# Kernel tuning notes

Hardware: AMD Instinct MI355X
Metric: run time of the kernel (lower is better)

Reference implementation:

```python
import jax, jax.numpy as jnp
import numpy as np

I, L, T, S = 128, 8, 128, 128   # input neurons, topo batches, neurons per batch, fan-in span
BIG = 1e9
EPS = 1e-5


def setup_inputs() -> dict:
    key = jax.random.key(0)
    ks = jax.random.split(key, 7)
    x = jax.random.normal(ks[0], (I,), jnp.float32)
    # per-neuron weights|bias, scaled down for numerical stability of softmax/gelu chain
    W = jax.random.normal(ks[1], (L, T, S + 1), jnp.float32) * 0.05
    mask = (jax.random.uniform(ks[2], (L, T, S)) > 0.5).astype(jnp.float32)  # DAG connectivity
    attn_t = jax.random.normal(ks[3], (L, 3, S, S + 1), jnp.float32) * 0.05      # topo q/k/v (weight|bias)
    attn_n = jax.random.normal(ks[4], (L, T, 3, S, S + 1), jnp.float32) * 0.05   # per-neuron q/k/v
    # additive attention mask: attend only over a neuron's actual inputs
    attn_mask_n = BIG * (1.0 - mask[:, :, :, None] * mask[:, :, None, :])        # (L,T,S,S)
    norm_params = jnp.stack([jnp.ones((L, S)), jnp.zeros((L, S))], 1) \
        + 0.1 * jax.random.normal(ks[5], (L, 2, S), jnp.float32)                 # gamma, beta
    ada = jnp.ones((L, T, 2), jnp.float32) \
        + 0.1 * jax.random.normal(ks[6], (L, T, 2), jnp.float32)                 # gain, amplification
    span_ids = jnp.arange(L * S, dtype=jnp.int32).reshape(L, S)    # gather indices per topo batch
    tb_ids = I + jnp.arange(L * T, dtype=jnp.int32).reshape(L, T)  # scatter indices per topo batch
    return dict(x=x, W=W, mask=mask, attn_t=attn_t, attn_n=attn_n,
                attn_mask_n=attn_mask_n, norm_params=norm_params, ada=ada,
                span_ids=span_ids, tb_ids=tb_ids)


def _attention(qkv, vals, amask):
    # qkv: (3, S, S+1) stacked query/key/value (weight|bias); vals: (S,)
    wq, bq = qkv[0, :, :-1], qkv[0, :, -1]
    wk, bk = qkv[1, :, :-1], qkv[1, :, -1]
    wv, bv = qkv[2, :, :-1], qkv[2, :, -1]
    q = wq @ vals + bq
    k = wk @ vals + bk
    v = wv @ vals + bv
    scores = jnp.outer(q, k) * jax.lax.rsqrt(jnp.float32(vals.shape[0])) - amask
    return jax.nn.softmax(scores) @ v + vals  # residual connection


def _forward(x, W, mask, attn_t, attn_n, attn_mask_n, norm_params, ada, span_ids, tb_ids):
    values = jnp.zeros((I + L * T,), x.dtype).at[jnp.arange(I)].set(x)
    for b in range(L):  # fixed, small topological batch order
        vals = values[span_ids[b]]                                  # gather fan-in span (S,)
        mu = jnp.mean(vals)
        var = jnp.var(vals)
        vals = (vals - mu) * jax.lax.rsqrt(var + EPS)               # topo norm (standardize)
        vals = vals * norm_params[b, 0] + norm_params[b, 1]
        vals = _attention(attn_t[b], vals, 0.0)                     # topo-level self-attention
        # neuron-level self-attention, vmapped over the batch's T neurons -> (T, S)
        vals_n = jax.vmap(_attention, in_axes=(0, None, 0))(attn_n[b], vals, attn_mask_n[b])
        w, bias = W[b, :, :-1], W[b, :, -1]
        aff = jnp.einsum('ts,ts->t', w * mask[b], vals_n) + bias    # masked affine per neuron
        if b == L - 1:
            out = aff                                               # output neurons: identity transform
        else:
            out = jax.nn.gelu(aff * ada[b, :, 0]) * ada[b, :, 1]    # adaptive activation a*sigma(b*x)
        values = values.at[tb_ids[b]].set(out)
    return values[tb_ids[L - 1]]


def reference(x, W, mask, attn_t, attn_n, attn_mask_n, norm_params, ada, span_ids, tb_ids):
    return _forward(x, W, mask, attn_t, attn_n, attn_mask_n, norm_params, ada, span_ids, tb_ids)
```

## Files before the change

### kernel.cpp

```cpp
#include <hip/hip_runtime.h>
#include <math.h>

#define L_DIM 8
#define T_DIM 128
#define S_DIM 128
#define SP1   129
#define NSTRIDE 132
#define BIGF  1000000000.0f
#define EPSF  1e-5f
#define NTHREADS 1024
#define NWAVES 16

template<int CTRL>
__device__ __forceinline__ float dpp_add_part(float x) {
    int r = __builtin_amdgcn_update_dpp(0, __float_as_int(x), CTRL, 0xF, 0xF, false);
    return __int_as_float(r);
}
__device__ __forceinline__ float dpp16Sum15(float x) {
    x += dpp_add_part<0x111>(x);
    x += dpp_add_part<0x112>(x);
    x += dpp_add_part<0x114>(x);
    x += dpp_add_part<0x118>(x);
    return x;
}
__device__ __forceinline__ float dppSum63(float x) {
    x += dpp_add_part<0x111>(x);
    x += dpp_add_part<0x112>(x);
    x += dpp_add_part<0x114>(x);
    x += dpp_add_part<0x118>(x);
    x += dpp_add_part<0x142>(x);
    x += dpp_add_part<0x143>(x);
    return x;
}
__device__ __forceinline__ float lane63(float x) {
    return __int_as_float(__builtin_amdgcn_readlane(__float_as_int(x), 63));
}

__device__ __forceinline__ void wg_bar() {
    asm volatile("s_waitcnt lgkmcnt(0)" ::: "memory");
    __builtin_amdgcn_s_barrier();
    asm volatile("" ::: "memory");
}

__device__ __forceinline__ void gld_lds4(const float* g, float* l) {
    __builtin_amdgcn_global_load_lds(
        (const __attribute__((address_space(1))) void*)g,
        (__attribute__((address_space(3))) void*)l,
        4, 0, 0);
}

__device__ __forceinline__ void mv_glb4(const float* __restrict__ mat,
                                        const float in[8], int li, int rb,
                                        float* __restrict__ dst) {
#pragma unroll
    for (int p = 0; p < 4; ++p) {
        int r = rb + 4 * p;
        const float* row = mat + (size_t)r * SP1;
        float acc = 0.0f;
#pragma unroll
        for (int e = 0; e < 8; ++e) acc = fmaf(row[li * 8 + e], in[e], acc);
        acc = dpp16Sum15(acc);
        if (li == 15) dst[r] = acc + row[128];
    }
}

__device__ __forceinline__ void mv_stage2(const float* __restrict__ mat,
                                          const float* __restrict__ biasArr,
                                          const float in[8], int li, int r_base,
                                          float* __restrict__ dst) {
#pragma unroll
    for (int p = 0; p < 2; ++p) {
        int r = r_base + p * 4;
        const float* row = mat + r * NSTRIDE;
        float acc = 0.0f;
#pragma unroll
        for (int e = 0; e < 8; ++e) acc = fmaf(row[li * 8 + e], in[e], acc);
        acc = dpp16Sum15(acc);
        if (li == 15) dst[r] = acc + biasArr[r];
    }
}

__device__ __forceinline__ void mv_regs(const float wv[2][8], const float wb[2],
                                        const float in[8], int li, int r_base,
                                        float* __restrict__ dst) {
#pragma unroll
    for (int p = 0; p < 2; ++p) {
        float acc = 0.0f;
#pragma unroll
        for (int e = 0; e < 8; ++e) acc = fmaf(wv[p][e], in[e], acc);
        acc = dpp16Sum15(acc);
        if (li == 15) dst[r_base + p * 4] = acc + wb[p];
    }
}

__device__ __forceinline__ void attn_sm_t(int li, int r_base,
                                          const float* __restrict__ lds_q,
                                          const float* __restrict__ lds_k,
                                          const float* __restrict__ lds_v,
                                          const float* __restrict__ resid,
                                          float* __restrict__ lds_out)
{
    const float scale = 0.08838834764831845f;
    float kx[8], vx[8];
#pragma unroll
    for (int e = 0; e < 8; ++e) { kx[e] = lds_k[li * 8 + e]; vx[e] = lds_v[li * 8 + e]; }
#pragma unroll
    for (int p = 0; p < 2; ++p) {
        int r = r_base + p * 4;
        float qs = lds_q[r] * scale;
        float den = 0.0f, num = 0.0f;
#pragma unroll
        for (int e = 0; e < 8; ++e) {
            float ee = __expf(qs * kx[e]);
            den += ee;
            num = fmaf(ee, vx[e], num);
        }
        den = dpp16Sum15(den);
        num = dpp16Sum15(num);
        if (li == 15) lds_out[r] = num / den + resid[r];
    }
}

__global__ __launch_bounds__(NTHREADS)
void net_kernel(const float* __restrict__ x,
                const float* __restrict__ W,
                const float* __restrict__ maskp,
                const float* __restrict__ attn_t,
                const float* __restrict__ attn_n,
                const float* __restrict__ norm_params,
                const float* __restrict__ ada,
                float* __restrict__ out,
                unsigned long long* __restrict__ mbox)
{
    const int t    = blockIdx.x;
    const int tid  = threadIdx.x;
    const int lane = tid & 63;
    const int wid  = tid >> 6;
    const int li   = lane & 15;
    const int g    = lane >> 4;
    const int r0   = wid * 8 + g;
    const int r1   = r0 + 4;

    __shared__ float lds_nq[S_DIM * NSTRIDE];
    __shared__ float lds_nk[S_DIM * NSTRIDE];
    __shared__ float lds_nqb[S_DIM], lds_nkb[S_DIM];
    __shared__ float lds_vals[S_DIM];
    __shared__ float lds_q[S_DIM], lds_k[S_DIM], lds_v[S_DIM];
    __shared__ float lds_tv[S_DIM];
    __shared__ float lds_aff[NWAVES];

    float nv[2][8];
    float nvb0, nvb1;

    {
        const float* srcn = attn_n + (size_t)t * 3 * S_DIM * SP1;
        if (wid >= 8) {
            if (wid == 8)  gld_lds4(srcn + (size_t)lane * SP1 + 128, lds_nqb);
            if (wid == 9)  gld_lds4(srcn + (size_t)(64 + lane) * SP1 + 128, lds_nqb + 64);
            if (wid == 10) gld_lds4(srcn + (size_t)(S_DIM + lane) * SP1 + 128, lds_nkb);
            if (wid == 11) gld_lds4(srcn + (size_t)(S_DIM + 64 + lane) * SP1 + 128, lds_nkb + 64);
            const float* kb_ = srcn + S_DIM * SP1;
#pragma unroll
            for (int k2 = 0; k2 < 16; ++k2) {
                int r = (wid - 8) + 8 * k2;
                gld_lds4(srcn + (size_t)r * SP1 + lane,      lds_nq + r * NSTRIDE);
                gld_lds4(srcn + (size_t)r * SP1 + 64 + lane, lds_nq + r * NSTRIDE + 64);
                gld_lds4(kb_  + (size_t)r * SP1 + lane,      lds_nk + r * NSTRIDE);
                gld_lds4(kb_  + (size_t)r * SP1 + 64 + lane, lds_nk + r * NSTRIDE + 64);
            }
        }
        const float* vb_ = srcn + 2 * S_DIM * SP1;
#pragma unroll
        for (int e = 0; e < 8; ++e) {
            nv[0][e] = vb_[(size_t)r0 * SP1 + li * 8 + e];
            nv[1][e] = vb_[(size_t)r1 * SP1 + li * 8 + e];
        }
        nvb0 = vb_[(size_t)r0 * SP1 + 128];
        nvb1 = vb_[(size_t)r1 * SP1 + 128];
    }

    for (int b = 0; b < L_DIM; ++b) {
        if (wid == 0) {
            float np00 = norm_params[(b * 2 + 0) * S_DIM + lane];
            float np10 = norm_params[(b * 2 + 0) * S_DIM + lane + 64];
            float np01 = norm_params[(b * 2 + 1) * S_DIM + lane];
            float np11 = norm_params[(b * 2 + 1) * S_DIM + lane + 64];
            float v0, v1;
            if (b == 0) {
                v0 = x[lane]; v1 = x[lane + 64];
            } else {
                float a00 = ada[((b - 1) * T_DIM + lane) * 2 + 0];
                float a01 = ada[((b - 1) * T_DIM + lane) * 2 + 1];
                float a10 = ada[((b - 1) * T_DIM + lane + 64) * 2 + 0];
                float a11 = ada[((b - 1) * T_DIM + lane + 64) * 2 + 1];
                const unsigned long long* mb_ = mbox + (size_t)(b - 1) * T_DIM;
                unsigned long long u0, u1;
                do {
                    u0 = __hip_atomic_load(&mb_[lane], __ATOMIC_RELAXED, __HIP_MEMORY_SCOPE_AGENT);
                    u1 = __hip_atomic_load(&mb_[lane + 64], __ATOMIC_RELAXED, __HIP_MEMORY_SCOPE_AGENT);
                } while ((unsigned int)(u0 >> 32) != (unsigned int)b ||
                         (unsigned int)(u1 >> 32) != (unsigned int)b);
                {
                    float z = __uint_as_float((unsigned int)u0) * a00;
                    float z3 = z * z * z;
                    v0 = 0.5f * z * (1.0f + tanhf(0.7978845608028654f * (z + 0.044715f * z3))) * a01;
                }
                {
                    float z = __uint_as_float((unsigned int)u1) * a10;
                    float z3 = z * z * z;
                    v1 = 0.5f * z * (1.0f + tanhf(0.7978845608028654f * (z + 0.044715f * z3))) * a11;
                }
            }
            float s  = dppSum63(v0 + v1);
            float mu = lane63(s) * (1.0f / 128.0f);
            float d0 = v0 - mu, d1 = v1 - mu;
            float s2 = dppSum63(fmaf(d0, d0, d1 * d1));
            float rstd = rsqrtf(lane63(s2) * (1.0f / 128.0f) + EPSF);
            lds_vals[lane]      = d0 * rstd * np00 + np01;
            lds_vals[lane + 64] = d1 * rstd * np10 + np11;
        }
        wg_bar();

        if (wid < 8) {
            float iv[8];
#pragma unroll
            for (int e = 0; e < 8; ++e) iv[e] = lds_vals[li * 8 + e];
            const float* bb = attn_t + (size_t)b * 3 * S_DIM * SP1;
            int rb = wid * 16 + g;
            mv_glb4(bb,                   iv, li, rb, lds_q);
            mv_glb4(bb + 1 * S_DIM * SP1, iv, li, rb, lds_k);
            mv_glb4(bb + 2 * S_DIM * SP1, iv, li, rb, lds_v);
        }
        wg_bar();

        attn_sm_t(li, r0, lds_q, lds_k, lds_v, lds_vals, lds_tv);
        if (wid >= 8) asm volatile("s_waitcnt vmcnt(0)" ::: "memory");
        wg_bar();

        const float* mrow = maskp + (size_t)(b * T_DIM + t) * S_DIM;
        const float* wrow = W + (size_t)(b * T_DIM + t) * SP1;
        float m1mj[8];
#pragma unroll
        for (int e = 0; e < 8; ++e) m1mj[e] = 1.0f - mrow[li * 8 + e];
        float mr0 = mrow[r0], mr1 = mrow[r1];
        float wr0 = wrow[r0], wr1 = wrow[r1];
        float wb  = (wid == 0) ? wrow[128] : 0.0f;

        {
            float tvv[8];
#pragma unroll
            for (int e = 0; e < 8; ++e) tvv[e] = lds_tv[li * 8 + e];
            mv_stage2(lds_nq, lds_nqb, tvv, li, r0, lds_q);
            mv_stage2(lds_nk, lds_nkb, tvv, li, r0, lds_k);
            float bv[2] = { nvb0, nvb1 };
            mv_regs(nv, bv, tvv, li, r0, lds_v);
        }
        wg_bar();

        if (b < L_DIM - 1) {
            const float* srcn = attn_n + (size_t)((b + 1) * T_DIM + t) * 3 * S_DIM * SP1;
            const float* mnx  = maskp + (size_t)((b + 1) * T_DIM + t) * S_DIM;
            float mr0n = mnx[r0], mr1n = mnx[r1];
            float mml = (wid >= 8 && lane < 16) ? mnx[(wid - 8) + 8 * lane] : 0.0f;
            unsigned long long bal = __ballot(mml != 0.0f);
            bool a0 = (mr0n != 0.0f), a1 = (mr1n != 0.0f);
            const float* vb_ = srcn + 2 * S_DIM * SP1;
            if (a0) {
#pragma unroll
                for (int e = 0; e < 8; ++e) nv[0][e] = vb_[(size_t)r0 * SP1 + li * 8 + e];
                nvb0 = vb_[(size_t)r0 * SP1 + 128];
            } else {
#pragma unroll
                for (int e = 0; e < 8; ++e) nv[0][e] = 0.0f;
                nvb0 = 0.0f;
            }
            if (a1) {
#pragma unroll
                for (int e = 0; e < 8; ++e) nv[1][e] = vb_[(size_t)r1 * SP1 + li * 8 + e];
                nvb1 = vb_[(size_t)r1 * SP1 + 128];
            } else {
#pragma unroll
                for (int e = 0; e < 8; ++e) nv[1][e] = 0.0f;
                nvb1 = 0.0f;
            }
            if (wid >= 8) {
                if (wid == 8)  gld_lds4(srcn + (size_t)lane * SP1 + 128, lds_nqb);
                if (wid == 9)  gld_lds4(srcn + (size_t)(64 + lane) * SP1 + 128, lds_nqb + 64);
                if (wid == 10) gld_lds4(srcn + (size_t)(S_DIM + lane) * SP1 + 128, lds_nkb);
                if (wid == 11) gld_lds4(srcn + (size_t)(S_DIM + 64 + lane) * SP1 + 128, lds_nkb + 64);
                const float* kb_ = srcn + S_DIM * SP1;
#pragma unroll
                for (int k2 = 0; k2 < 16; ++k2) {
                    if ((bal >> k2) & 1ull) {
                        int r = (wid - 8) + 8 * k2;
                        gld_lds4(srcn + (size_t)r * SP1 + lane,      lds_nq + r * NSTRIDE);
                        gld_lds4(srcn + (size_t)r * SP1 + 64 + lane, lds_nq + r * NSTRIDE + 64);
                        gld_lds4(kb_  + (size_t)r * SP1 + lane,      lds_nk + r * NSTRIDE);
                        gld_lds4(kb_  + (size_t)r * SP1 + 64 + lane, lds_nk + r * NSTRIDE + 64);
                    }
                }
            }
        }

        {
            const float scale = 0.08838834764831845f;
            float kx[8], vx[8];
#pragma unroll
            for (int e = 0; e < 8; ++e) { kx[e] = lds_k[li * 8 + e]; vx[e] = lds_v[li * 8 + e]; }
            float o0 = 0.0f, o1 = 0.0f;
#pragma unroll
            for (int p = 0; p < 2; ++p) {
                int r = r0 + p * 4;
                float mrp = p ? mr1 : mr0;
                float qv = lds_q[r];
                float qs = (mrp == 0.0f) ? 0.0f : qv * scale;
                float bp = BIGF * mrp;
                float den = 0.0f, num = 0.0f;
#pragma unroll
                for (int e = 0; e < 8; ++e) {
                    float s_ = fmaf(-bp, m1mj[e], qs * kx[e]);
                    float ee = __expf(s_);
                    den += ee;
                    num = fmaf(ee, vx[e], num);
                }
                den = dpp16Sum15(den);
                num = dpp16Sum15(num);
                float o = num / den + lds_tv[r];
                if (p) o1 = o; else o0 = o;
            }
            float part = (li == 15) ? (wr0 * mr0 * o0 + wr1 * mr1 * o1) : 0.0f;
            part = dppSum63(part);
            if (lane == 63) lds_aff[wid] = part;
        }
        wg_bar();

        if (wid == 0) {
            float pa = (lane < NWAVES) ? lds_aff[lane] : 0.0f;
            pa = dppSum63(pa);
            if (lane == 63) {
                float aff = pa + wb;
                if (b == L_DIM - 1) {
                    out[t] = aff;
                } else {
                    unsigned long long u =
                        ((unsigned long long)(unsigned int)(b + 1) << 32) |
                        (unsigned long long)__float_as_uint(aff);
                    __hip_atomic_store(&mbox[(size_t)b * T_DIM + t], u,
                                       __ATOMIC_RELAXED, __HIP_MEMORY_SCOPE_AGENT);
                }
            }
        }
    }
}

extern "C" void kernel_launch(void* const* d_in, const int* in_sizes, int n_in,
                              void* d_out, int out_size, void* d_ws, size_t ws_size,
                              hipStream_t stream) {
    const float* x           = (const float*)d_in[0];
    const float* W           = (const float*)d_in[1];
    const float* maskp       = (const float*)d_in[2];
    const float* attn_t      = (const float*)d_in[3];
    const float* attn_n      = (const float*)d_in[4];
    const float* norm_params = (const float*)d_in[6];
    const float* ada         = (const float*)d_in[7];
    float* out = (float*)d_out;

    unsigned long long* mbox = (unsigned long long*)d_ws;

    hipMemsetAsync(d_ws, 0, (size_t)(L_DIM - 1) * T_DIM * sizeof(unsigned long long), stream);

    void* args[] = { (void*)&x, (void*)&W, (void*)&maskp, (void*)&attn_t, (void*)&attn_n,
                     (void*)&norm_params, (void*)&ada, (void*)&out, (void*)&mbox };
    hipLaunchCooperativeKernel((const void*)net_kernel, dim3(T_DIM), dim3(NTHREADS),
                               args, 0, stream);
}
```

Baseline: 466.6 us.

## Stage neuron q/k weights with 16-byte swizzled LDS loads across all waves

Per-neuron q/k weight rows now go into LDS through 16-byte global_load_lds transfers from all 16 waves. They use a dense 128-float row layout with an XOR swizzle, replacing 4-byte loads from 8 waves into a padded stride, and reads use float4. The topo-level matvec now runs on all waves with 2 rows each instead of 8 waves with 4 rows. Mask and weight row loads move to the top of each batch iteration, and the separate vmcnt wait is folded into one barrier. The changes aim to cut the number of load instructions and the LDS bank conflicts, at the cost of making every wave wait on its outstanding loads at that barrier. One concern is that the 16-byte loads read rows with a 129-float stride, which may be unaligned.

```diff
diff --git a/kernel.cpp b/kernel.cpp
--- a/kernel.cpp
+++ b/kernel.cpp
@@ -5,7 +5,6 @@
 #define T_DIM 128
 #define S_DIM 128
 #define SP1   129
-#define NSTRIDE 132
 #define BIGF  1000000000.0f
 #define EPSF  1e-5f
 #define NTHREADS 1024
@@ -41,7 +40,18 @@
     __builtin_amdgcn_s_barrier();
     asm volatile("" ::: "memory");
 }
-
+__device__ __forceinline__ void wg_bar_vm() {
+    asm volatile("s_waitcnt vmcnt(0) lgkmcnt(0)" ::: "memory");
+    __builtin_amdgcn_s_barrier();
+    asm volatile("" ::: "memory");
+}
+
+__device__ __forceinline__ void gld_lds16(const float* g, float* l) {
+    __builtin_amdgcn_global_load_lds(
+        (const __attribute__((address_space(1))) void*)g,
+        (__attribute__((address_space(3))) void*)l,
+        16, 0, 0);
+}
 __device__ __forceinline__ void gld_lds4(const float* g, float* l) {
     __builtin_amdgcn_global_load_lds(
         (const __attribute__((address_space(1))) void*)g,
@@ -49,12 +59,20 @@
         4, 0, 0);
 }
 
-__device__ __forceinline__ void mv_glb4(const float* __restrict__ mat,
-                                        const float in[8], int li, int rb,
-                                        float* __restrict__ dst) {
-#pragma unroll
-    for (int p = 0; p < 4; ++p) {
-        int r = rb + 4 * p;
+__device__ __forceinline__ void stage_pair(const float* __restrict__ src,
+                                           float* __restrict__ lds, int c, int lane) {
+    int r  = 2 * c + (lane >> 5);
+    int lb = ((lane & 31) * 16) ^ ((r & 7) << 4);
+    gld_lds16((const float*)((const char*)(src + (size_t)r * SP1) + lb),
+              lds + c * 256);
+}
+
+__device__ __forceinline__ void mv_glb(const float* __restrict__ mat,
+                                       const float in[8], int li, int r_base,
+                                       float* __restrict__ dst) {
+#pragma unroll
+    for (int p = 0; p < 2; ++p) {
+        int r = r_base + p * 4;
         const float* row = mat + (size_t)r * SP1;
         float acc = 0.0f;
 #pragma unroll
@@ -64,17 +82,22 @@
     }
 }
 
-__device__ __forceinline__ void mv_stage2(const float* __restrict__ mat,
-                                          const float* __restrict__ biasArr,
-                                          const float in[8], int li, int r_base,
-                                          float* __restrict__ dst) {
+__device__ __forceinline__ void mv_stage_swz(const float* __restrict__ mat,
+                                             const float* __restrict__ biasArr,
+                                             const float in[8], int li, int r_base,
+                                             float* __restrict__ dst) {
 #pragma unroll
     for (int p = 0; p < 2; ++p) {
         int r = r_base + p * 4;
-        const float* row = mat + r * NSTRIDE;
+        const char* rowp = (const char*)(mat + (size_t)r * 128);
+        int swz = (r & 7) << 4;
+        const float4 a = *(const float4*)(rowp + (((li * 32)     ) ^ swz));
+        const float4 b = *(const float4*)(rowp + (((li * 32) + 16) ^ swz));
         float acc = 0.0f;
-#pragma unroll
-        for (int e = 0; e < 8; ++e) acc = fmaf(row[li * 8 + e], in[e], acc);
+        acc = fmaf(a.x, in[0], acc); acc = fmaf(a.y, in[1], acc);
+        acc = fmaf(a.z, in[2], acc); acc = fmaf(a.w, in[3], acc);
+        acc = fmaf(b.x, in[4], acc); acc = fmaf(b.y, in[5], acc);
+        acc = fmaf(b.z, in[6], acc); acc = fmaf(b.w, in[7], acc);
         acc = dpp16Sum15(acc);
         if (li == 15) dst[r] = acc + biasArr[r];
     }
@@ -141,8 +164,8 @@
     const int r0   = wid * 8 + g;
     const int r1   = r0 + 4;
 
-    __shared__ float lds_nq[S_DIM * NSTRIDE];
-    __shared__ float lds_nk[S_DIM * NSTRIDE];
+    __shared__ float lds_nq[S_DIM * 128];
+    __shared__ float lds_nk[S_DIM * 128];
     __shared__ float lds_nqb[S_DIM], lds_nkb[S_DIM];
     __shared__ float lds_vals[S_DIM];
     __shared__ float lds_q[S_DIM], lds_k[S_DIM], lds_v[S_DIM];
@@ -154,20 +177,16 @@
 
     {
         const float* srcn = attn_n + (size_t)t * 3 * S_DIM * SP1;
-        if (wid >= 8) {
-            if (wid == 8)  gld_lds4(srcn + (size_t)lane * SP1 + 128, lds_nqb);
-            if (wid == 9)  gld_lds4(srcn + (size_t)(64 + lane) * SP1 + 128, lds_nqb + 64);
-            if (wid == 10) gld_lds4(srcn + (size_t)(S_DIM + lane) * SP1 + 128, lds_nkb);
-            if (wid == 11) gld_lds4(srcn + (size_t)(S_DIM + 64 + lane) * SP1 + 128, lds_nkb + 64);
-            const float* kb_ = srcn + S_DIM * SP1;
-#pragma unroll
-            for (int k2 = 0; k2 < 16; ++k2) {
-                int r = (wid - 8) + 8 * k2;
-                gld_lds4(srcn + (size_t)r * SP1 + lane,      lds_nq + r * NSTRIDE);
-                gld_lds4(srcn + (size_t)r * SP1 + 64 + lane, lds_nq + r * NSTRIDE + 64);
-                gld_lds4(kb_  + (size_t)r * SP1 + lane,      lds_nk + r * NSTRIDE);
-                gld_lds4(kb_  + (size_t)r * SP1 + 64 + lane, lds_nk + r * NSTRIDE + 64);
-            }
+        const float* kb_  = srcn + S_DIM * SP1;
+        if (wid == 12) gld_lds4(srcn + (size_t)lane * SP1 + 128, lds_nqb);
+        if (wid == 13) gld_lds4(srcn + (size_t)(64 + lane) * SP1 + 128, lds_nqb + 64);
+        if (wid == 14) gld_lds4(kb_  + (size_t)lane * SP1 + 128, lds_nkb);
+        if (wid == 15) gld_lds4(kb_  + (size_t)(64 + lane) * SP1 + 128, lds_nkb + 64);
+#pragma unroll
+        for (int k2 = 0; k2 < 4; ++k2) {
+            int c = wid + 16 * k2;
+            stage_pair(srcn, lds_nq, c, lane);
+            stage_pair(kb_,  lds_nk, c, lane);
         }
         const float* vb_ = srcn + 2 * S_DIM * SP1;
 #pragma unroll
@@ -180,6 +199,15 @@
     }
 
     for (int b = 0; b < L_DIM; ++b) {
+        const float* mrow = maskp + (size_t)(b * T_DIM + t) * S_DIM;
+        const float* wrow = W + (size_t)(b * T_DIM + t) * SP1;
+        float m1mj[8];
+#pragma unroll
+        for (int e = 0; e < 8; ++e) m1mj[e] = 1.0f - mrow[li * 8 + e];
+        float mr0 = mrow[r0], mr1 = mrow[r1];
+        float wr0 = wrow[r0], wr1 = wrow[r1];
+        float wb  = (wid == 0) ? wrow[128] : 0.0f;
+
         if (wid == 0) {
             float np00 = norm_params[(b * 2 + 0) * S_DIM + lane];
             float np10 = norm_params[(b * 2 + 0) * S_DIM + lane + 64];
@@ -221,37 +249,26 @@
         }
         wg_bar();
 
-        if (wid < 8) {
+        {
             float iv[8];
 #pragma unroll
             for (int e = 0; e < 8; ++e) iv[e] = lds_vals[li * 8 + e];
             const float* bb = attn_t + (size_t)b * 3 * S_DIM * SP1;
-            int rb = wid * 16 + g;
-            mv_glb4(bb,                   iv, li, rb, lds_q);
-            mv_glb4(bb + 1 * S_DIM * SP1, iv, li, rb, lds_k);
-            mv_glb4(bb + 2 * S_DIM * SP1, iv, li, rb, lds_v);
+            mv_glb(bb,                    iv, li, r0, lds_q);
+            mv_glb(bb + 1 * S_DIM * SP1,  iv, li, r0, lds_k);
+            mv_glb(bb + 2 * S_DIM * SP1,  iv, li, r0, lds_v);
         }
         wg_bar();
 
         attn_sm_t(li, r0, lds_q, lds_k, lds_v, lds_vals, lds_tv);
-        if (wid >= 8) asm volatile("s_waitcnt vmcnt(0)" ::: "memory");
-        wg_bar();
-
-        const float* mrow = maskp + (size_t)(b * T_DIM + t) * S_DIM;
-        const float* wrow = W + (size_t)(b * T_DIM + t) * SP1;
-        float m1mj[8];
-#pragma unroll
-        for (int e = 0; e < 8; ++e) m1mj[e] = 1.0f - mrow[li * 8 + e];
-        float mr0 = mrow[r0], mr1 = mrow[r1];
-        float wr0 = wrow[r0], wr1 = wrow[r1];
-        float wb  = (wid == 0) ? wrow[128] : 0.0f;
+        wg_bar_vm();
 
         {
             float tvv[8];
 #pragma unroll
             for (int e = 0; e < 8; ++e) tvv[e] = lds_tv[li * 8 + e];
-            mv_stage2(lds_nq, lds_nqb, tvv, li, r0, lds_q);
-            mv_stage2(lds_nk, lds_nkb, tvv, li, r0, lds_k);
+            mv_stage_swz(lds_nq, lds_nqb, tvv, li, r0, lds_q);
+            mv_stage_swz(lds_nk, lds_nkb, tvv, li, r0, lds_k);
             float bv[2] = { nvb0, nvb1 };
             mv_regs(nv, bv, tvv, li, r0, lds_v);
         }
@@ -261,8 +278,8 @@
             const float* srcn = attn_n + (size_t)((b + 1) * T_DIM + t) * 3 * S_DIM * SP1;
             const float* mnx  = maskp + (size_t)((b + 1) * T_DIM + t) * S_DIM;
             float mr0n = mnx[r0], mr1n = mnx[r1];
-            float mml = (wid >= 8 && lane < 16) ? mnx[(wid - 8) + 8 * lane] : 0.0f;
-            unsigned long long bal = __ballot(mml != 0.0f);
+            bool pa = (mnx[2 * lane] != 0.0f) || (mnx[2 * lane + 1] != 0.0f);
+            unsigned long long bal = __ballot(pa);
             bool a0 = (mr0n != 0.0f), a1 = (mr1n != 0.0f);
             const float* vb_ = srcn + 2 * S_DIM * SP1;
             if (a0) {
@@ -283,21 +300,17 @@
                 for (int e = 0; e < 8; ++e) nv[1][e] = 0.0f;
                 nvb1 = 0.0f;
             }
-            if (wid >= 8) {
-                if (wid == 8)  gld_lds4(srcn + (size_t)lane * SP1 + 128, lds_nqb);
-                if (wid == 9)  gld_lds4(srcn + (size_t)(64 + lane) * SP1 + 128, lds_nqb + 64);
-                if (wid == 10) gld_lds4(srcn + (size_t)(S_DIM + lane) * SP1 + 128, lds_nkb);
-                if (wid == 11) gld_lds4(srcn + (size_t)(S_DIM + 64 + lane) * SP1 + 128, lds_nkb + 64);
-                const float* kb_ = srcn + S_DIM * SP1;
-#pragma unroll
-                for (int k2 = 0; k2 < 16; ++k2) {
-                    if ((bal >> k2) & 1ull) {
-                        int r = (wid - 8) + 8 * k2;
-                        gld_lds4(srcn + (size_t)r * SP1 + lane,      lds_nq + r * NSTRIDE);
-                        gld_lds4(srcn + (size_t)r * SP1 + 64 + lane, lds_nq + r * NSTRIDE + 64);
-                        gld_lds4(kb_  + (size_t)r * SP1 + lane,      lds_nk + r * NSTRIDE);
-                        gld_lds4(kb_  + (size_t)r * SP1 + 64 + lane, lds_nk + r * NSTRIDE + 64);
-                    }
+            const float* kb_ = srcn + S_DIM * SP1;
+            if (wid == 12) gld_lds4(srcn + (size_t)lane * SP1 + 128, lds_nqb);
+            if (wid == 13) gld_lds4(srcn + (size_t)(64 + lane) * SP1 + 128, lds_nqb + 64);
+            if (wid == 14) gld_lds4(kb_  + (size_t)lane * SP1 + 128, lds_nkb);
+            if (wid == 15) gld_lds4(kb_  + (size_t)(64 + lane) * SP1 + 128, lds_nkb + 64);
+#pragma unroll
+            for (int k2 = 0; k2 < 4; ++k2) {
+                int c = wid + 16 * k2;
+                if ((bal >> c) & 1ull) {
+                    stage_pair(srcn, lds_nq, c, lane);
+                    stage_pair(kb_,  lds_nk, c, lane);
                 }
             }
         }
@@ -335,10 +348,10 @@
         wg_bar();
 
         if (wid == 0) {
-            float pa = (lane < NWAVES) ? lds_aff[lane] : 0.0f;
-            pa = dppSum63(pa);
+            float pa2 = (lane < NWAVES) ? lds_aff[lane] : 0.0f;
+            pa2 = dppSum63(pa2);
             if (lane == 63) {
-                float aff = pa + wb;
+                float aff = pa2 + wb;
                 if (b == L_DIM - 1) {
                     out[t] = aff;
                 } else {
```

After: 422.5 us. -9.4%, faster.
